# Optimization experiments

Hardware: AMD Instinct MI355X
Metric: run time of the kernel (lower is better)

The kernel has to match this reference:

```python
import jax, jax.numpy as jnp
import numpy as np

B, L, E, H = 4, 2048, 1024, 16
HD = E // H  # head_dim = 64


def setup_inputs() -> dict:
    key = jax.random.key(0)
    ks = jax.random.split(key, 11)
    s = 1.0 / np.sqrt(E)
    return {
        "q": jax.random.normal(ks[0], (B, L, E), jnp.float32),
        "k": jax.random.normal(ks[1], (B, L, E), jnp.float32),
        "v": jax.random.normal(ks[2], (B, L, E), jnp.float32),
        "Wq": jax.random.normal(ks[3], (E, E), jnp.float32) * s,
        "bq": jax.random.normal(ks[4], (E,), jnp.float32) * s,
        "Wk": jax.random.normal(ks[5], (E, E), jnp.float32) * s,
        "bk": jax.random.normal(ks[6], (E,), jnp.float32) * s,
        "Wv": jax.random.normal(ks[7], (E, E), jnp.float32) * s,
        "bv": jax.random.normal(ks[8], (E,), jnp.float32) * s,
        "Wo": jax.random.normal(ks[9], (E, E), jnp.float32) * s,
        "bo": jax.random.normal(ks[10], (E,), jnp.float32) * s,
    }


def reference(q, k, v, Wq, bq, Wk, bk, Wv, bv, Wo, bo):
    # Linear projections (torch Linear: x @ W.T + b)
    qp = q @ Wq.T + bq  # [B, L, E]
    kp = k @ Wk.T + bk
    vp = v @ Wv.T + bv
    # split heads -> [B, H, L, HD]
    qh = qp.reshape(B, L, H, HD).transpose(0, 2, 1, 3)
    kh = kp.reshape(B, L, H, HD).transpose(0, 2, 1, 3)
    vh = vp.reshape(B, L, H, HD).transpose(0, 2, 1, 3)
    scale = 1.0 / jnp.sqrt(jnp.asarray(HD, qh.dtype))
    score = jnp.einsum("bhqd,bhkd->bhqk", qh, kh) * scale  # [B, H, L, L]
    attn = jax.nn.softmax(score, axis=-1)
    # dropout p=0 (eval) -> identity
    out = jnp.einsum("bhqk,bhkd->bhqd", attn, vh)  # [B, H, L, HD]
    out = out.transpose(0, 2, 1, 3).reshape(B, L, E)
    out = out @ Wo.T + bo
    # original returns attn flattened over (B*H); match that shape
    return out, attn.reshape(B * H, L, L)
```

## Files before the change

### kernel.cpp

```cpp
#include <hip/hip_runtime.h>
#include <stdint.h>

typedef __attribute__((ext_vector_type(8))) short bf16x8;
typedef __attribute__((ext_vector_type(4))) float f32x4;

#define DEV __device__ __forceinline__

static constexpr int Bsz = 4, Lsz = 2048, Esz = 1024, Hsz = 16, HDsz = 64;
static constexpr int BL = Bsz * Lsz;
static constexpr size_t PLANE = (size_t)BL * Esz;

DEV unsigned short f2bf(float x) {
  union { float f; unsigned u; } c; c.f = x;
  unsigned u = c.u + 0x7FFFu + ((c.u >> 16) & 1u);
  return (unsigned short)(u >> 16);
}
DEV float bf2f(unsigned short h) {
  union { unsigned u; float f; } c; c.u = ((unsigned)h) << 16; return c.f;
}
DEV bf16x8 ld_bf8(const unsigned short* p) { return *(const bf16x8*)p; }

template<bool A_F32, bool W_SPLIT, bool OUT_F32>
__global__ __launch_bounds__(256) void gemm_nt(
    const void* __restrict__ Aptr, const float* __restrict__ W,
    const float* __restrict__ bias, void* __restrict__ Cptr)
{
  constexpr int Kdim = Esz, Ndim = Esz;
  __shared__ unsigned short As[128][40];
  __shared__ unsigned short Bs[W_SPLIT ? 2 : 1][128][40];

  const int t = threadIdx.x;
  const int lane = t & 63, wave = t >> 6;
  const int wr = wave >> 1, wc = wave & 1;
  const int frow = lane & 15, fg = lane >> 4;

  const int f = blockIdx.x + 8 * blockIdx.y;
  const int m_t = ((f & 7) << 3) + (f >> 6);
  const int n_t = (f >> 3) & 7;
  const int m0 = m_t * 128, n0 = n_t * 128;

  f32x4 acc[4][4];
#pragma unroll
  for (int i = 0; i < 4; i++)
#pragma unroll
    for (int j = 0; j < 4; j++) acc[i][j] = f32x4{0.f, 0.f, 0.f, 0.f};

  for (int k0 = 0; k0 < Kdim; k0 += 32) {
    __syncthreads();
#pragma unroll
    for (int j = 0; j < 4; j++) {
      int s = t + j * 256, row = s >> 3, c4 = s & 7;
      if constexpr (A_F32) {
        const float* A = (const float*)Aptr;
        float4 v = *(const float4*)&A[(size_t)(m0 + row) * Kdim + k0 + c4 * 4];
        ushort4 hi;
        hi.x = f2bf(v.x); hi.y = f2bf(v.y); hi.z = f2bf(v.z); hi.w = f2bf(v.w);
        *(ushort4*)&As[row][c4 * 4] = hi;
      } else {
        const unsigned short* A = (const unsigned short*)Aptr;
        *(ushort4*)&As[row][c4 * 4] =
            *(const ushort4*)&A[(size_t)(m0 + row) * Kdim + k0 + c4 * 4];
      }
      {
        float4 v = *(const float4*)&W[(size_t)(n0 + row) * Kdim + k0 + c4 * 4];
        ushort4 hi;
        hi.x = f2bf(v.x); hi.y = f2bf(v.y); hi.z = f2bf(v.z); hi.w = f2bf(v.w);
        *(ushort4*)&Bs[0][row][c4 * 4] = hi;
        if constexpr (W_SPLIT) {
          ushort4 lo;
          lo.x = f2bf(v.x - bf2f(hi.x));
          lo.y = f2bf(v.y - bf2f(hi.y));
          lo.z = f2bf(v.z - bf2f(hi.z));
          lo.w = f2bf(v.w - bf2f(hi.w));
          *(ushort4*)&Bs[W_SPLIT ? 1 : 0][row][c4 * 4] = lo;
        }
      }
    }
    __syncthreads();

    bf16x8 ah[4], bhv[4], blv[4];
#pragma unroll
    for (int x = 0; x < 4; x++) {
      ah[x] = ld_bf8(&As[wr * 64 + x * 16 + frow][fg * 8]);
      bhv[x] = ld_bf8(&Bs[0][wc * 64 + x * 16 + frow][fg * 8]);
      if constexpr (W_SPLIT)
        blv[x] = ld_bf8(&Bs[W_SPLIT ? 1 : 0][wc * 64 + x * 16 + frow][fg * 8]);
    }
#pragma unroll
    for (int mi = 0; mi < 4; mi++)
#pragma unroll
      for (int ni = 0; ni < 4; ni++) {
        acc[mi][ni] = __builtin_amdgcn_mfma_f32_16x16x32_bf16(ah[mi], bhv[ni], acc[mi][ni], 0, 0, 0);
        if constexpr (W_SPLIT)
          acc[mi][ni] = __builtin_amdgcn_mfma_f32_16x16x32_bf16(ah[mi], blv[ni], acc[mi][ni], 0, 0, 0);
      }
  }

#pragma unroll
  for (int mi = 0; mi < 4; mi++)
#pragma unroll
    for (int ni = 0; ni < 4; ni++) {
      int col = n0 + wc * 64 + ni * 16 + frow;
      float bv = bias[col];
#pragma unroll
      for (int r = 0; r < 4; r++) {
        int row = m0 + wr * 64 + mi * 16 + fg * 4 + r;
        float val = acc[mi][ni][r] + bv;
        size_t idx = (size_t)row * Ndim + col;
        if constexpr (OUT_F32) ((float*)Cptr)[idx] = val;
        else                   ((unsigned short*)Cptr)[idx] = f2bf(val);
      }
    }
}

__global__ __launch_bounds__(256) void attn_fused(
    const unsigned short* __restrict__ qph, const unsigned short* __restrict__ kph,
    const unsigned short* __restrict__ vp,
    float* __restrict__ attn, unsigned short* __restrict__ oh)
{
  __shared__ unsigned short QP[64][72];
  __shared__ unsigned short Kh[64][72];
  __shared__ unsigned short Vt[64][72];

  const int t = threadIdx.x, lane = t & 63, wave = t >> 6;
  const int frow = lane & 15, fg = lane >> 4;

  const int f = blockIdx.x + 32 * blockIdx.y;
  const int bh = ((f & 7) << 3) + (f >> 8);
  const int qt = (f >> 3) & 31;
  const int b = bh >> 4, h = bh & 15;
  const int q0 = qt * 64;
  const int qw = q0 + wave * 16;

  const size_t base = (size_t)b * Lsz * Esz + (size_t)h * HDsz;
  constexpr float SC2 = 0.1803368801f;

  const int srow = t >> 4, sc4 = (t & 15) * 4;
  const int vrow = t >> 4, vc = t & 15;

  auto loadKh = [&](ushort4* r, int row0) {
#pragma unroll
    for (int j = 0; j < 4; j++)
      r[j] = *(const ushort4*)&kph[base + (size_t)(row0 + srow + j * 16) * Esz + sc4];
  };
  auto writeK = [&](unsigned short (*dst)[72], const ushort4* r) {
#pragma unroll
    for (int j = 0; j < 4; j++)
      *(ushort4*)&dst[srow + j * 16][sc4] = r[j];
  };
  auto loadV = [&](unsigned short (*rv)[4], int row0) {
#pragma unroll
    for (int j = 0; j < 4; j++) {
      size_t g = base + (size_t)(row0 + vrow + j * 16) * Esz + vc;
#pragma unroll
      for (int i = 0; i < 4; i++) rv[j][i] = vp[g + i * 16];
    }
  };
  auto writeV = [&](unsigned short (*rv)[4]) {
#pragma unroll
    for (int j = 0; j < 4; j++) {
#pragma unroll
      for (int i = 0; i < 4; i++) Vt[vc + i * 16][vrow + j * 16] = rv[j][i];
    }
  };

#pragma unroll
  for (int j = 0; j < 4; j++) {
    size_t g = base + (size_t)(q0 + srow + j * 16) * Esz + sc4;
    *(ushort4*)&QP[srow + j * 16][sc4] = *(const ushort4*)&qph[g];
  }
  __syncthreads();
  bf16x8 qfh[2];
#pragma unroll
  for (int dh = 0; dh < 2; dh++)
    qfh[dh] = ld_bf8(&QP[wave * 16 + frow][dh * 32 + fg * 8]);

  float zl[4];
#pragma unroll
  for (int r = 0; r < 4; r++) zl[r] = 0.f;

  auto computeA = [&](unsigned short (*Kc)[72]) {
#pragma unroll
    for (int kc = 0; kc < 4; kc++) {
      f32x4 sv = f32x4{0.f, 0.f, 0.f, 0.f};
#pragma unroll
      for (int dh = 0; dh < 2; dh++) {
        bf16x8 kf = ld_bf8(&Kc[kc * 16 + frow][dh * 32 + fg * 8]);
        sv = __builtin_amdgcn_mfma_f32_16x16x32_bf16(qfh[dh], kf, sv, 0, 0, 0);
      }
#pragma unroll
      for (int r = 0; r < 4; r++) zl[r] += exp2f(sv[r] * SC2);
    }
  };

  {
    ushort4 rA[4], rB[4];
    loadKh(rA, 0);
    loadKh(rB, 64);
    for (int kt = 0; kt < 32; kt += 2) {
      __syncthreads();
      writeK(Kh, rA);
      writeK(Vt, rB);
      if (kt + 2 < 32) {
        loadKh(rA, (kt + 2) * 64);
        loadKh(rB, (kt + 3) * 64);
      }
      __syncthreads();
      computeA(Kh);
      computeA(Vt);
    }
  }
  float rz[4];
#pragma unroll
  for (int r = 0; r < 4; r++) {
    float z = zl[r];
#pragma unroll
    for (int o = 1; o < 16; o <<= 1) z += __shfl_xor(z, o);
    rz[r] = 1.f / z;
  }

  f32x4 oacc[4];
#pragma unroll
  for (int d = 0; d < 4; d++) oacc[d] = f32x4{0.f, 0.f, 0.f, 0.f};

  const size_t arow = (size_t)bh * Lsz * Lsz;

  auto computeB = [&](int kt) {
    f32x4 sv[4];
#pragma unroll
    for (int kc = 0; kc < 4; kc++) {
      sv[kc] = f32x4{0.f, 0.f, 0.f, 0.f};
#pragma unroll
      for (int dh = 0; dh < 2; dh++) {
        bf16x8 kfh = ld_bf8(&Kh[kc * 16 + frow][dh * 32 + fg * 8]);
        sv[kc] = __builtin_amdgcn_mfma_f32_16x16x32_bf16(qfh[dh], kfh, sv[kc], 0, 0, 0);
      }
    }
#pragma unroll
    for (int kc = 0; kc < 4; kc++) {
#pragma unroll
      for (int r = 0; r < 4; r++) {
        float p = exp2f(sv[kc][r] * SC2) * rz[r];
        QP[wave * 16 + fg * 4 + r][kc * 16 + frow] = f2bf(p);
      }
    }
    __syncthreads();
#pragma unroll
    for (int it = 0; it < 4; it++) {
      int prow = it * 4 + fg;
      int pc = frow * 4;
      ushort4 pv4 = *(const ushort4*)&QP[wave * 16 + prow][pc];
      f32x4 w;
      w[0] = bf2f(pv4.x); w[1] = bf2f(pv4.y); w[2] = bf2f(pv4.z); w[3] = bf2f(pv4.w);
      __builtin_nontemporal_store(w,
          (f32x4*)&attn[arow + (size_t)(qw + prow) * Lsz + kt * 64 + pc]);
    }
#pragma unroll
    for (int kh2 = 0; kh2 < 2; kh2++) {
      bf16x8 pa = ld_bf8(&QP[wave * 16 + frow][kh2 * 32 + fg * 8]);
#pragma unroll
      for (int d = 0; d < 4; d++) {
        bf16x8 vb = ld_bf8(&Vt[d * 16 + frow][kh2 * 32 + fg * 8]);
        oacc[d] = __builtin_amdgcn_mfma_f32_16x16x32_bf16(pa, vb, oacc[d], 0, 0, 0);
      }
    }
  };

  {
    ushort4 khA[4], khB[4];
    unsigned short vA[4][4], vB[4][4];
    loadKh(khA, 0);
    loadV(vA, 0);
    for (int kt = 0; kt < 32; kt += 2) {
      __syncthreads();
      writeK(Kh, khA);
      writeV(vA);
      if (kt + 1 < 32) {
        loadKh(khB, (kt + 1) * 64);
        loadV(vB, (kt + 1) * 64);
      }
      __syncthreads();
      computeB(kt);
      __syncthreads();
      writeK(Kh, khB);
      writeV(vB);
      if (kt + 2 < 32) {
        loadKh(khA, (kt + 2) * 64);
        loadV(vA, (kt + 2) * 64);
      }
      __syncthreads();
      computeB(kt + 1);
    }
  }

#pragma unroll
  for (int d = 0; d < 4; d++)
#pragma unroll
    for (int r = 0; r < 4; r++) {
      int qrow = qw + fg * 4 + r;
      __builtin_nontemporal_store(f2bf(oacc[d][r]),
          &oh[base + (size_t)qrow * Esz + d * 16 + frow]);
    }
}

extern "C" void kernel_launch(void* const* d_in, const int* in_sizes, int n_in,
                              void* d_out, int out_size, void* d_ws, size_t ws_size,
                              hipStream_t stream)
{
  (void)in_sizes; (void)n_in; (void)out_size; (void)ws_size;

  const float* q  = (const float*)d_in[0];
  const float* k  = (const float*)d_in[1];
  const float* v  = (const float*)d_in[2];
  const float* Wq = (const float*)d_in[3];
  const float* bq = (const float*)d_in[4];
  const float* Wk = (const float*)d_in[5];
  const float* bk = (const float*)d_in[6];
  const float* Wv = (const float*)d_in[7];
  const float* bv = (const float*)d_in[8];
  const float* Wo = (const float*)d_in[9];
  const float* bo = (const float*)d_in[10];

  float* out  = (float*)d_out;
  float* attn = out + PLANE;

  unsigned short* qph = (unsigned short*)d_ws;
  unsigned short* kph = qph + PLANE;
  unsigned short* vpp = kph + PLANE;
  unsigned short* oh  = vpp + PLANE;

  dim3 gg(8, 64), bb(256);
  gemm_nt<true, false, false><<<gg, bb, 0, stream>>>(q, Wq, bq, qph);
  gemm_nt<true, false, false><<<gg, bb, 0, stream>>>(k, Wk, bk, kph);
  gemm_nt<true, false, false><<<gg, bb, 0, stream>>>(v, Wv, bv, vpp);

  dim3 ga(32, 64);
  attn_fused<<<ga, bb, 0, stream>>>(qph, kph, vpp, attn, oh);

  gemm_nt<false, true, true><<<gg, bb, 0, stream>>>(oh, Wo, bo, out);
}
```

Measured before the change: 475.1 us.

## Batch QKV projections into one launch and drop Wo hi/lo split

Merges the three input projection GEMMs into a single launch with a z grid dimension that selects q/k/v pointers, cutting launch overhead and letting the three projections share the GPU concurrently. The output projection no longer splits Wo into bf16 hi and lo parts, which halves its MFMA count and shared-memory use at some cost in accuracy. The fp32 output store becomes nontemporal to avoid cache pollution.

After: 463.5 us. 2.4% less time.

```diff
diff --git a/kernel.cpp b/kernel.cpp
--- a/kernel.cpp
+++ b/kernel.cpp
@@ -20,15 +20,12 @@
 }
 DEV bf16x8 ld_bf8(const unsigned short* p) { return *(const bf16x8*)p; }
 
-template<bool A_F32, bool W_SPLIT, bool OUT_F32>
-__global__ __launch_bounds__(256) void gemm_nt(
-    const void* __restrict__ Aptr, const float* __restrict__ W,
-    const float* __restrict__ bias, void* __restrict__ Cptr)
+template<bool A_F32, bool OUT_F32>
+DEV void gemm_body(const void* __restrict__ Aptr, const float* __restrict__ W,
+                   const float* __restrict__ bias, void* __restrict__ Cptr,
+                   unsigned short (*As)[40], unsigned short (*Bs)[40])
 {
   constexpr int Kdim = Esz, Ndim = Esz;
-  __shared__ unsigned short As[128][40];
-  __shared__ unsigned short Bs[W_SPLIT ? 2 : 1][128][40];
-
   const int t = threadIdx.x;
   const int lane = t & 63, wave = t >> 6;
   const int wr = wave >> 1, wc = wave & 1;
@@ -65,35 +62,22 @@
         float4 v = *(const float4*)&W[(size_t)(n0 + row) * Kdim + k0 + c4 * 4];
         ushort4 hi;
         hi.x = f2bf(v.x); hi.y = f2bf(v.y); hi.z = f2bf(v.z); hi.w = f2bf(v.w);
-        *(ushort4*)&Bs[0][row][c4 * 4] = hi;
-        if constexpr (W_SPLIT) {
-          ushort4 lo;
-          lo.x = f2bf(v.x - bf2f(hi.x));
-          lo.y = f2bf(v.y - bf2f(hi.y));
-          lo.z = f2bf(v.z - bf2f(hi.z));
-          lo.w = f2bf(v.w - bf2f(hi.w));
-          *(ushort4*)&Bs[W_SPLIT ? 1 : 0][row][c4 * 4] = lo;
-        }
+        *(ushort4*)&Bs[row][c4 * 4] = hi;
       }
     }
     __syncthreads();
 
-    bf16x8 ah[4], bhv[4], blv[4];
+    bf16x8 ah[4], bhv[4];
 #pragma unroll
     for (int x = 0; x < 4; x++) {
       ah[x] = ld_bf8(&As[wr * 64 + x * 16 + frow][fg * 8]);
-      bhv[x] = ld_bf8(&Bs[0][wc * 64 + x * 16 + frow][fg * 8]);
-      if constexpr (W_SPLIT)
-        blv[x] = ld_bf8(&Bs[W_SPLIT ? 1 : 0][wc * 64 + x * 16 + frow][fg * 8]);
+      bhv[x] = ld_bf8(&Bs[wc * 64 + x * 16 + frow][fg * 8]);
     }
 #pragma unroll
     for (int mi = 0; mi < 4; mi++)
 #pragma unroll
-      for (int ni = 0; ni < 4; ni++) {
+      for (int ni = 0; ni < 4; ni++)
         acc[mi][ni] = __builtin_amdgcn_mfma_f32_16x16x32_bf16(ah[mi], bhv[ni], acc[mi][ni], 0, 0, 0);
-        if constexpr (W_SPLIT)
-          acc[mi][ni] = __builtin_amdgcn_mfma_f32_16x16x32_bf16(ah[mi], blv[ni], acc[mi][ni], 0, 0, 0);
-      }
   }
 
 #pragma unroll
@@ -107,10 +91,36 @@
         int row = m0 + wr * 64 + mi * 16 + fg * 4 + r;
         float val = acc[mi][ni][r] + bv;
         size_t idx = (size_t)row * Ndim + col;
-        if constexpr (OUT_F32) ((float*)Cptr)[idx] = val;
-        else                   ((unsigned short*)Cptr)[idx] = f2bf(val);
-      }
-    }
+        if constexpr (OUT_F32)
+          __builtin_nontemporal_store(val, &((float*)Cptr)[idx]);
+        else
+          ((unsigned short*)Cptr)[idx] = f2bf(val);
+      }
+    }
+}
+
+__global__ __launch_bounds__(256) void gemm_proj3(
+    const float* qA, const float* kA, const float* vA,
+    const float* Wq, const float* Wk, const float* Wv,
+    const float* bq, const float* bk, const float* bv,
+    unsigned short* qC, unsigned short* kC, unsigned short* vC)
+{
+  __shared__ unsigned short As[128][40];
+  __shared__ unsigned short Bs[128][40];
+  const int z = blockIdx.z;
+  const float* A = z == 0 ? qA : (z == 1 ? kA : vA);
+  const float* W = z == 0 ? Wq : (z == 1 ? Wk : Wv);
+  const float* bias = z == 0 ? bq : (z == 1 ? bk : bv);
+  unsigned short* C = z == 0 ? qC : (z == 1 ? kC : vC);
+  gemm_body<true, false>(A, W, bias, C, As, Bs);
+}
+
+__global__ __launch_bounds__(256) void gemm_out(
+    const unsigned short* A, const float* W, const float* bias, float* C)
+{
+  __shared__ unsigned short As[128][40];
+  __shared__ unsigned short Bs[128][40];
+  gemm_body<false, true>(A, W, bias, C, As, Bs);
 }
 
 __global__ __launch_bounds__(256) void attn_fused(
@@ -329,13 +339,12 @@
   unsigned short* vpp = kph + PLANE;
   unsigned short* oh  = vpp + PLANE;
 
-  dim3 gg(8, 64), bb(256);
-  gemm_nt<true, false, false><<<gg, bb, 0, stream>>>(q, Wq, bq, qph);
-  gemm_nt<true, false, false><<<gg, bb, 0, stream>>>(k, Wk, bk, kph);
-  gemm_nt<true, false, false><<<gg, bb, 0, stream>>>(v, Wv, bv, vpp);
+  dim3 bb(256);
+  gemm_proj3<<<dim3(8, 64, 3), bb, 0, stream>>>(q, k, v, Wq, Wk, Wv,
+                                                bq, bk, bv, qph, kph, vpp);
 
   dim3 ga(32, 64);
   attn_fused<<<ga, bb, 0, stream>>>(qph, kph, vpp, attn, oh);
 
-  gemm_nt<false, true, true><<<gg, bb, 0, stream>>>(oh, Wo, bo, out);
-}
+  gemm_out<<<dim3(8, 64), bb, 0, stream>>>(oh, Wo, bo, out);
+}
```
